# Performance work log

Measured on AMD Instinct MI355X. Metric: run time of the kernel, lower is better.

The kernel has to match this reference:

```python
import jax, jax.numpy as jnp
import numpy as np

DECAY = 0.99
BETA = 0.25
EPS_NORM = 1e-12  # matches F.normalize eps


def _l2_normalize(x):
    n = jnp.linalg.norm(x, axis=-1, keepdims=True)
    return x / jnp.maximum(n, EPS_NORM)


def setup_inputs() -> dict:
    key = jax.random.key(0)
    ks = jax.random.split(key, 8)
    B, C, H, W = 16, 256, 64, 64
    D, K = 16, 4096  # codebook_dim, n_embed
    z = jax.random.normal(ks[0], (B, C, H, W), dtype=jnp.float32)
    # 1x1 convs == per-pixel linear layers
    w_down = jax.random.normal(ks[1], (D, C), dtype=jnp.float32) / np.sqrt(C).astype(np.float32)
    b_down = jnp.zeros((D,), dtype=jnp.float32)
    w_up = jax.random.normal(ks[2], (C, D), dtype=jnp.float32) / np.sqrt(D).astype(np.float32)
    b_up = jnp.zeros((C,), dtype=jnp.float32)
    embedding = jax.random.uniform(ks[3], (K, D), minval=-1.0 / K, maxval=1.0 / K, dtype=jnp.float32)
    cluster_size = jax.random.uniform(ks[4], (K,), minval=0.5, maxval=2.0, dtype=jnp.float32)
    embed_avg = jax.random.normal(ks[5], (K, D), dtype=jnp.float32) * 0.01
    return {"z": z, "w_down": w_down, "b_down": b_down, "w_up": w_up,
            "b_up": b_up, "embedding": embedding,
            "cluster_size": cluster_size, "embed_avg": embed_avg}


def reference(z, w_down, b_down, w_up, b_up, embedding, cluster_size, embed_avg):
    B, C, H, W = z.shape
    K, D = embedding.shape

    # proj_down: 1x1 conv -> per-token linear
    z_low = jnp.einsum('bchw,dc->bdhw', z, w_down) + b_down[None, :, None, None]
    z_flat = z_low.transpose(0, 2, 3, 1).reshape(-1, D)          # [N, D]
    z_norm = _l2_normalize(z_flat)
    e_norm = _l2_normalize(embedding)                             # [K, D]

    # squared L2 distances (argmin identical to cdist argmin)
    d2 = (jnp.sum(z_norm * z_norm, -1, keepdims=True)
          - 2.0 * z_norm @ e_norm.T
          + jnp.sum(e_norm * e_norm, -1)[None, :])               # [N, K]
    indices = jnp.argmin(d2, axis=-1)                             # [N]
    z_q_flat = e_norm[indices]                                    # [N, D]

    # EMA buffer update (training path); scatter-accumulate via segment_sum
    ones = jnp.ones(indices.shape, dtype=jnp.float32)
    batch_cluster_size = jax.ops.segment_sum(ones, indices, num_segments=K)
    batch_embed_sum = jax.ops.segment_sum(z_norm, indices, num_segments=K)
    new_cluster_size = cluster_size * DECAY + (1.0 - DECAY) * batch_cluster_size
    new_embed_avg = embed_avg * DECAY + (1.0 - DECAY) * batch_embed_sum
    n = new_cluster_size.sum()
    cs = (new_cluster_size + 1e-5) / (n + K * 1e-5) * n
    new_embedding = new_embed_avg / cs[:, None]

    commitment_loss = BETA * jnp.mean((z_norm - jax.lax.stop_gradient(z_q_flat)) ** 2)

    # straight-through estimator
    z_q_low_flat = z_norm + jax.lax.stop_gradient(z_q_flat - z_norm)
    z_q_low = z_q_low_flat.reshape(B, H, W, D).transpose(0, 3, 1, 2)
    z_q = jnp.einsum('bdhw,cd->bchw', z_q_low, w_up) + b_up[None, :, None, None]

    indices_2d = indices.reshape(B, H, W)

    # metrics / entropy loss (usage == bincount(indices))
    usage_prob = batch_cluster_size / (batch_cluster_size.sum() + 1e-8)
    entropy = -jnp.sum(usage_prob * jnp.log(usage_prob + 1e-8))
    entropy_loss = jnp.log(jnp.float32(K)) - entropy

    return (z_q, commitment_loss, indices_2d, entropy_loss,
            new_embedding, new_cluster_size, new_embed_avg)
```

## Files before the change

### kernel.cpp

```cpp
#include <hip/hip_runtime.h>
#include <math.h>

#define NTOK 65536
#define CDIM 256
#define DDIM 16
#define KCOD 4096
#define HWSZ 4096

#define KSPLIT 16
#define CPS (KCOD / KSPLIT)
#define TPT 8
#define TBLK (256 * TPT)

#define WS_ENORM 0
#define WS_ENN   (WS_ENORM + KCOD*DDIM)
#define WS_ZN    (WS_ENN + KCOD)
#define WS_ZNN   (WS_ZN + NTOK*DDIM)
#define WS_BCS   (WS_ZNN + NTOK)
#define WS_BES   (WS_BCS + KCOD)
#define WS_SCAL  (WS_BES + KCOD*DDIM)
#define WS_PACK  (WS_SCAL + 8)

#define OFS_ZQ   0
#define OFS_LOSS 16777216
#define OFS_IDX  16777217
#define OFS_ENT  16842753
#define OFS_NE   16842754
#define OFS_NCS  16908290
#define OFS_NEA  16912386

__global__ __launch_bounds__(256) void knorm_kernel(const float* __restrict__ emb,
                                                    float* __restrict__ ws) {
  int k = blockIdx.x * 256 + threadIdx.x;
  const float4* src = (const float4*)emb + (size_t)k * 4;
  float4 t0 = src[0], t1 = src[1], t2 = src[2], t3 = src[3];
  float e[16] = {t0.x,t0.y,t0.z,t0.w, t1.x,t1.y,t1.z,t1.w,
                 t2.x,t2.y,t2.z,t2.w, t3.x,t3.y,t3.z,t3.w};
  float ss = 0.f;
  #pragma unroll
  for (int d = 0; d < 16; ++d) ss += e[d] * e[d];
  float dn = fmaxf(sqrtf(ss), 1e-12f);
  #pragma unroll
  for (int d = 0; d < 16; ++d) e[d] = e[d] / dn;
  float s2 = 0.f;
  #pragma unroll
  for (int d = 0; d < 16; ++d) s2 += e[d] * e[d];
  float4* dst = (float4*)(ws + WS_ENORM) + (size_t)k * 4;
  dst[0] = make_float4(e[0],e[1],e[2],e[3]);
  dst[1] = make_float4(e[4],e[5],e[6],e[7]);
  dst[2] = make_float4(e[8],e[9],e[10],e[11]);
  dst[3] = make_float4(e[12],e[13],e[14],e[15]);
  ws[WS_ENN + k] = s2;
}

__global__ __launch_bounds__(256) void kdown_kernel(const float* __restrict__ z,
                                                    const float* __restrict__ w_down,
                                                    const float* __restrict__ b_down,
                                                    float* __restrict__ ws) {
  __shared__ float wdT[CDIM * DDIM];
  const int tid = threadIdx.x;
  const int n = blockIdx.x * 256 + tid;
  const int b = n >> 12;
  const int hw = n & 4095;

  for (int i = tid; i < CDIM * DDIM; i += 256) {
    int d = i >> 8, c = i & 255;
    wdT[c * 16 + d] = w_down[i];
  }
  __syncthreads();

  const float* zp = z + (size_t)b * (CDIM * HWSZ) + hw;
  float acc[16];
  #pragma unroll
  for (int d = 0; d < 16; ++d) acc[d] = 0.f;
  #pragma unroll 16
  for (int c = 0; c < CDIM; ++c) {
    float zv = zp[(size_t)c * HWSZ];
    const float4* wr = (const float4*)(wdT + c * 16);
    float4 w0 = wr[0], w1 = wr[1], w2 = wr[2], w3 = wr[3];
    acc[0]  = fmaf(zv, w0.x, acc[0]);  acc[1]  = fmaf(zv, w0.y, acc[1]);
    acc[2]  = fmaf(zv, w0.z, acc[2]);  acc[3]  = fmaf(zv, w0.w, acc[3]);
    acc[4]  = fmaf(zv, w1.x, acc[4]);  acc[5]  = fmaf(zv, w1.y, acc[5]);
    acc[6]  = fmaf(zv, w1.z, acc[6]);  acc[7]  = fmaf(zv, w1.w, acc[7]);
    acc[8]  = fmaf(zv, w2.x, acc[8]);  acc[9]  = fmaf(zv, w2.y, acc[9]);
    acc[10] = fmaf(zv, w2.z, acc[10]); acc[11] = fmaf(zv, w2.w, acc[11]);
    acc[12] = fmaf(zv, w3.x, acc[12]); acc[13] = fmaf(zv, w3.y, acc[13]);
    acc[14] = fmaf(zv, w3.z, acc[14]); acc[15] = fmaf(zv, w3.w, acc[15]);
  }
  #pragma unroll
  for (int d = 0; d < 16; ++d) acc[d] = acc[d] + b_down[d];
  float ss = 0.f;
  #pragma unroll
  for (int d = 0; d < 16; ++d) ss += acc[d] * acc[d];
  float dn = fmaxf(sqrtf(ss), 1e-12f);
  float zn[16];
  #pragma unroll
  for (int d = 0; d < 16; ++d) zn[d] = acc[d] / dn;
  float znn = 0.f;
  {
    float sq[16];
    #pragma unroll
    for (int d = 0; d < 16; ++d) sq[d] = zn[d] * zn[d];
    #pragma unroll
    for (int d = 0; d < 16; ++d) znn += sq[d];
  }
  float4* op = (float4*)(ws + WS_ZN) + (size_t)n * 4;
  op[0] = make_float4(zn[0],zn[1],zn[2],zn[3]);
  op[1] = make_float4(zn[4],zn[5],zn[6],zn[7]);
  op[2] = make_float4(zn[8],zn[9],zn[10],zn[11]);
  op[3] = make_float4(zn[12],zn[13],zn[14],zn[15]);
  ws[WS_ZNN + n] = znn;
}

__global__ __launch_bounds__(256) void kscan_kernel(float* __restrict__ ws) {
  __shared__ float ecache[CPS * DDIM];
  __shared__ float encache[CPS];

  const int tid = threadIdx.x;
  const int kbase = blockIdx.y * CPS;

  {
    const float4* s4 = (const float4*)(ws + WS_ENORM + (size_t)kbase * 16);
    float4* d4 = (float4*)ecache;
    #pragma unroll
    for (int i = 0; i < 4; ++i) d4[tid + i * 256] = s4[tid + i * 256];
    encache[tid] = ws[WS_ENN + kbase + tid];
  }
  __syncthreads();

  float zn[TPT][16];
  float znn[TPT], best[TPT];
  int bidx[TPT];
  const int tokbase = blockIdx.x * TBLK + tid;
  {
    const float4* zp = (const float4*)(ws + WS_ZN);
    #pragma unroll
    for (int p = 0; p < TPT; ++p) {
      int tok = tokbase + p * 256;
      float4 a0 = zp[(size_t)tok * 4 + 0];
      float4 a1 = zp[(size_t)tok * 4 + 1];
      float4 a2 = zp[(size_t)tok * 4 + 2];
      float4 a3 = zp[(size_t)tok * 4 + 3];
      zn[p][0]=a0.x; zn[p][1]=a0.y; zn[p][2]=a0.z; zn[p][3]=a0.w;
      zn[p][4]=a1.x; zn[p][5]=a1.y; zn[p][6]=a1.z; zn[p][7]=a1.w;
      zn[p][8]=a2.x; zn[p][9]=a2.y; zn[p][10]=a2.z; zn[p][11]=a2.w;
      zn[p][12]=a3.x; zn[p][13]=a3.y; zn[p][14]=a3.z; zn[p][15]=a3.w;
      znn[p] = ws[WS_ZNN + tok];
      best[p] = 3.4e38f;
      bidx[p] = 0;
    }
  }

  #pragma unroll 2
  for (int j = 0; j < CPS; ++j) {
    const float4* e4 = (const float4*)(ecache + j * 16);
    float4 c0 = e4[0], c1 = e4[1], c2 = e4[2], c3 = e4[3];
    float en = encache[j];
    #pragma unroll
    for (int p = 0; p < TPT; ++p) {
      float d = 0.f;
      d = fmaf(zn[p][0],  c0.x, d); d = fmaf(zn[p][1],  c0.y, d);
      d = fmaf(zn[p][2],  c0.z, d); d = fmaf(zn[p][3],  c0.w, d);
      d = fmaf(zn[p][4],  c1.x, d); d = fmaf(zn[p][5],  c1.y, d);
      d = fmaf(zn[p][6],  c1.z, d); d = fmaf(zn[p][7],  c1.w, d);
      d = fmaf(zn[p][8],  c2.x, d); d = fmaf(zn[p][9],  c2.y, d);
      d = fmaf(zn[p][10], c2.z, d); d = fmaf(zn[p][11], c2.w, d);
      d = fmaf(zn[p][12], c3.x, d); d = fmaf(zn[p][13], c3.y, d);
      d = fmaf(zn[p][14], c3.z, d); d = fmaf(zn[p][15], c3.w, d);
      float sc = fmaf(-2.0f, d, znn[p]) + en;
      if (sc < best[p]) { best[p] = sc; bidx[p] = j; }
    }
  }

  unsigned long long* packp = (unsigned long long*)(ws + WS_PACK);
  #pragma unroll
  for (int p = 0; p < TPT; ++p) {
    int tok = tokbase + p * 256;
    unsigned u = __float_as_uint(best[p]);
    u = (u & 0x80000000u) ? ~u : (u | 0x80000000u);
    unsigned long long key =
        ((unsigned long long)u << 32) | (unsigned)(kbase + bidx[p]);
    atomicMin(packp + tok, key);
  }
}

__global__ __launch_bounds__(256) void kfinal_kernel(const float* __restrict__ w_up,
                                                     const float* __restrict__ b_up,
                                                     float* __restrict__ ws,
                                                     float* __restrict__ out) {
  __shared__ float wu[CDIM * DDIM];
  __shared__ float bu[CDIM];
  const int tid = threadIdx.x;
  {
    const float4* s4 = (const float4*)w_up;
    float4* d4 = (float4*)wu;
    #pragma unroll
    for (int i = 0; i < 4; ++i) d4[tid + i * 256] = s4[tid + i * 256];
    bu[tid] = b_up[tid];
  }
  __syncthreads();

  const int n = blockIdx.x * 256 + tid;
  const unsigned long long* packp = (const unsigned long long*)(ws + WS_PACK);
  const int bidx = (int)(unsigned)(packp[n] & 0xFFFFFFFFull);

  float zn[16];
  {
    const float4* zp = (const float4*)(ws + WS_ZN) + (size_t)n * 4;
    float4 a0 = zp[0], a1 = zp[1], a2 = zp[2], a3 = zp[3];
    zn[0]=a0.x; zn[1]=a0.y; zn[2]=a0.z; zn[3]=a0.w;
    zn[4]=a1.x; zn[5]=a1.y; zn[6]=a1.z; zn[7]=a1.w;
    zn[8]=a2.x; zn[9]=a2.y; zn[10]=a2.z; zn[11]=a2.w;
    zn[12]=a3.x; zn[13]=a3.y; zn[14]=a3.z; zn[15]=a3.w;
  }
  float zq[16];
  {
    const float4* eb = (const float4*)(ws + WS_ENORM) + (size_t)bidx * 4;
    float4 q0 = eb[0], q1 = eb[1], q2 = eb[2], q3 = eb[3];
    zq[0]=q0.x; zq[1]=q0.y; zq[2]=q0.z; zq[3]=q0.w;
    zq[4]=q1.x; zq[5]=q1.y; zq[6]=q1.z; zq[7]=q1.w;
    zq[8]=q2.x; zq[9]=q2.y; zq[10]=q2.z; zq[11]=q2.w;
    zq[12]=q3.x; zq[13]=q3.y; zq[14]=q3.z; zq[15]=q3.w;
  }

  out[OFS_IDX + n] = (float)bidx;

  float ls = 0.f;
  #pragma unroll
  for (int d = 0; d < 16; ++d) { float df = zn[d] - zq[d]; ls = fmaf(df, df, ls); }

  atomicAdd(ws + WS_BCS + bidx, 1.0f);
  #pragma unroll
  for (int d = 0; d < 16; ++d) atomicAdd(ws + WS_BES + (size_t)bidx * 16 + d, zn[d]);

  #pragma unroll
  for (int off = 32; off > 0; off >>= 1) ls += __shfl_down(ls, off, 64);
  if ((tid & 63) == 0) atomicAdd(ws + WS_SCAL + 0, ls);

  float ql[16];
  #pragma unroll
  for (int d = 0; d < 16; ++d) ql[d] = zn[d] + (zq[d] - zn[d]);

  const int b = n >> 12, hw = n & 4095;
  float* op = out + OFS_ZQ + (size_t)b * (CDIM * HWSZ) + hw;
  #pragma unroll 4
  for (int c = 0; c < CDIM; ++c) {
    const float4* wr = (const float4*)(wu + c * 16);
    float4 w0 = wr[0], w1 = wr[1], w2 = wr[2], w3 = wr[3];
    float a = 0.f;
    a = fmaf(ql[0],  w0.x, a); a = fmaf(ql[1],  w0.y, a);
    a = fmaf(ql[2],  w0.z, a); a = fmaf(ql[3],  w0.w, a);
    a = fmaf(ql[4],  w1.x, a); a = fmaf(ql[5],  w1.y, a);
    a = fmaf(ql[6],  w1.z, a); a = fmaf(ql[7],  w1.w, a);
    a = fmaf(ql[8],  w2.x, a); a = fmaf(ql[9],  w2.y, a);
    a = fmaf(ql[10], w2.z, a); a = fmaf(ql[11], w2.w, a);
    a = fmaf(ql[12], w3.x, a); a = fmaf(ql[13], w3.y, a);
    a = fmaf(ql[14], w3.z, a); a = fmaf(ql[15], w3.w, a);
    a = a + bu[c];
    op[(size_t)c * HWSZ] = a;
  }
}

__global__ __launch_bounds__(256) void kema_kernel(const float* __restrict__ cluster_size,
                                                   const float* __restrict__ embed_avg,
                                                   float* __restrict__ ws,
                                                   float* __restrict__ out) {
  const float DEC = 0.99f;
  const float OMD = (float)(1.0 - 0.99);
  const int k = blockIdx.x * 256 + threadIdx.x;
  float bcsv = ws[WS_BCS + k];
  float ncs = cluster_size[k] * DEC + OMD * bcsv;
  out[OFS_NCS + k] = ncs;
  #pragma unroll
  for (int d = 0; d < 16; ++d) {
    float nea = embed_avg[(size_t)k * 16 + d] * DEC + OMD * ws[WS_BES + (size_t)k * 16 + d];
    out[OFS_NEA + (size_t)k * 16 + d] = nea;
  }
  float p = bcsv / 65536.0f;
  float et = -p * logf(p + 1e-8f);

  __shared__ float r1[4], r2[4];
  float v1 = ncs, v2 = et;
  #pragma unroll
  for (int off = 32; off > 0; off >>= 1) {
    v1 += __shfl_down(v1, off, 64);
    v2 += __shfl_down(v2, off, 64);
  }
  int lane = threadIdx.x & 63, w = threadIdx.x >> 6;
  if (lane == 0) { r1[w] = v1; r2[w] = v2; }
  __syncthreads();
  if (threadIdx.x == 0) {
    atomicAdd(ws + WS_SCAL + 1, (r1[0] + r1[1]) + (r1[2] + r1[3]));
    atomicAdd(ws + WS_SCAL + 2, (r2[0] + r2[1]) + (r2[2] + r2[3]));
  }
}

__global__ __launch_bounds__(64) void kscal_kernel(const float* __restrict__ ws,
                                                   float* __restrict__ out) {
  if (threadIdx.x == 0) {
    out[OFS_LOSS] = 0.25f * (ws[WS_SCAL + 0] / 1048576.0f);
    out[OFS_ENT]  = (float)8.317766166719343 - ws[WS_SCAL + 2];
  }
}

__global__ __launch_bounds__(256) void kemb_kernel(const float* __restrict__ ws,
                                                   float* __restrict__ out) {
  const float KEPS = (float)(4096.0 * 1e-5);
  const int k = blockIdx.x * 256 + threadIdx.x;
  float n = ws[WS_SCAL + 1];
  float ncs = out[OFS_NCS + k];
  float cs = (ncs + 1e-5f) / (n + KEPS) * n;
  #pragma unroll
  for (int d = 0; d < 16; ++d)
    out[OFS_NE + (size_t)k * 16 + d] = out[OFS_NEA + (size_t)k * 16 + d] / cs;
}

extern "C" void kernel_launch(void* const* d_in, const int* in_sizes, int n_in,
                              void* d_out, int out_size, void* d_ws, size_t ws_size,
                              hipStream_t stream) {
  const float* z        = (const float*)d_in[0];
  const float* w_down   = (const float*)d_in[1];
  const float* b_down   = (const float*)d_in[2];
  const float* w_up     = (const float*)d_in[3];
  const float* b_up     = (const float*)d_in[4];
  const float* emb      = (const float*)d_in[5];
  const float* csz      = (const float*)d_in[6];
  const float* eavg     = (const float*)d_in[7];
  float* out = (float*)d_out;
  float* ws  = (float*)d_ws;

  hipMemsetAsync(ws + WS_BCS, 0, (size_t)(KCOD + KCOD*DDIM + 8) * sizeof(float), stream);
  hipMemsetAsync(ws + WS_PACK, 0xFF, (size_t)NTOK * 8, stream);

  knorm_kernel<<<KCOD / 256, 256, 0, stream>>>(emb, ws);
  kdown_kernel<<<NTOK / 256, 256, 0, stream>>>(z, w_down, b_down, ws);
  kscan_kernel<<<dim3(NTOK / TBLK, KSPLIT), 256, 0, stream>>>(ws);
  kfinal_kernel<<<NTOK / 256, 256, 0, stream>>>(w_up, b_up, ws, out);
  kema_kernel<<<KCOD / 256, 256, 0, stream>>>(csz, eavg, ws, out);
  kscal_kernel<<<1, 64, 0, stream>>>(ws, out);
  kemb_kernel<<<KCOD / 256, 256, 0, stream>>>(ws, out);
}
```

Before: 247.9 us.

## Restructure VQ kernels: drop shared staging, fold -2 and norm into scan, merge scalar kernel

The w_down transpose moves into the codebook-normalize kernel and is stored in workspace, so the down-projection reads it from global/cached memory and no longer stages it through LDS with a barrier. The w_up LDS staging in the final kernel is likewise removed. The scan kernel drops the per-token norm term, which is constant across codes and does not change the argmin, and pre-scales z by -2 so the distance becomes a single FMA chain seeded with the code norm. Tokens per thread drop from 8 to 4 with a launch_bounds occupancy hint, and the tiny scalar kernel is merged into the embedding kernel to save a launch. The main risk is that lower register reuse per thread in the scan, or uncoalesced broadcast global reads in place of LDS, could cost more than they save.

After: 271.6 us. +9.5%, slower.

```diff
diff --git a/kernel.cpp b/kernel.cpp
--- a/kernel.cpp
+++ b/kernel.cpp
@@ -9,14 +9,14 @@
 
 #define KSPLIT 16
 #define CPS (KCOD / KSPLIT)
-#define TPT 8
+#define TPT 4
 #define TBLK (256 * TPT)
 
 #define WS_ENORM 0
 #define WS_ENN   (WS_ENORM + KCOD*DDIM)
-#define WS_ZN    (WS_ENN + KCOD)
-#define WS_ZNN   (WS_ZN + NTOK*DDIM)
-#define WS_BCS   (WS_ZNN + NTOK)
+#define WS_WDT   (WS_ENN + KCOD)
+#define WS_ZN    (WS_WDT + CDIM*DDIM)
+#define WS_BCS   (WS_ZN + NTOK*DDIM)
 #define WS_BES   (WS_BCS + KCOD)
 #define WS_SCAL  (WS_BES + KCOD*DDIM)
 #define WS_PACK  (WS_SCAL + 8)
@@ -30,6 +30,7 @@
 #define OFS_NEA  16912386
 
 __global__ __launch_bounds__(256) void knorm_kernel(const float* __restrict__ emb,
+                                                    const float* __restrict__ w_down,
                                                     float* __restrict__ ws) {
   int k = blockIdx.x * 256 + threadIdx.x;
   const float4* src = (const float4*)emb + (size_t)k * 4;
@@ -51,32 +52,26 @@
   dst[2] = make_float4(e[8],e[9],e[10],e[11]);
   dst[3] = make_float4(e[12],e[13],e[14],e[15]);
   ws[WS_ENN + k] = s2;
+  ws[WS_WDT + k] = w_down[(k & 15) * 256 + (k >> 4)];
 }
 
 __global__ __launch_bounds__(256) void kdown_kernel(const float* __restrict__ z,
-                                                    const float* __restrict__ w_down,
+                                                    const float* __restrict__ wdt,
                                                     const float* __restrict__ b_down,
-                                                    float* __restrict__ ws) {
-  __shared__ float wdT[CDIM * DDIM];
+                                                    float* __restrict__ znp) {
   const int tid = threadIdx.x;
   const int n = blockIdx.x * 256 + tid;
   const int b = n >> 12;
   const int hw = n & 4095;
 
-  for (int i = tid; i < CDIM * DDIM; i += 256) {
-    int d = i >> 8, c = i & 255;
-    wdT[c * 16 + d] = w_down[i];
-  }
-  __syncthreads();
-
   const float* zp = z + (size_t)b * (CDIM * HWSZ) + hw;
   float acc[16];
   #pragma unroll
   for (int d = 0; d < 16; ++d) acc[d] = 0.f;
-  #pragma unroll 16
+  #pragma unroll 8
   for (int c = 0; c < CDIM; ++c) {
     float zv = zp[(size_t)c * HWSZ];
-    const float4* wr = (const float4*)(wdT + c * 16);
+    const float4* wr = (const float4*)(wdt + c * 16);
     float4 w0 = wr[0], w1 = wr[1], w2 = wr[2], w3 = wr[3];
     acc[0]  = fmaf(zv, w0.x, acc[0]);  acc[1]  = fmaf(zv, w0.y, acc[1]);
     acc[2]  = fmaf(zv, w0.z, acc[2]);  acc[3]  = fmaf(zv, w0.w, acc[3]);
@@ -96,23 +91,18 @@
   float zn[16];
   #pragma unroll
   for (int d = 0; d < 16; ++d) zn[d] = acc[d] / dn;
-  float znn = 0.f;
-  {
-    float sq[16];
-    #pragma unroll
-    for (int d = 0; d < 16; ++d) sq[d] = zn[d] * zn[d];
-    #pragma unroll
-    for (int d = 0; d < 16; ++d) znn += sq[d];
-  }
-  float4* op = (float4*)(ws + WS_ZN) + (size_t)n * 4;
+
+  float4* op = (float4*)znp + (size_t)n * 4;
   op[0] = make_float4(zn[0],zn[1],zn[2],zn[3]);
   op[1] = make_float4(zn[4],zn[5],zn[6],zn[7]);
   op[2] = make_float4(zn[8],zn[9],zn[10],zn[11]);
   op[3] = make_float4(zn[12],zn[13],zn[14],zn[15]);
-  ws[WS_ZNN + n] = znn;
-}
-
-__global__ __launch_bounds__(256) void kscan_kernel(float* __restrict__ ws) {
+}
+
+__global__ __launch_bounds__(256, 4) void kscan_kernel(const float* __restrict__ enorm,
+                                                       const float* __restrict__ ennp,
+                                                       const float* __restrict__ znp,
+                                                       unsigned long long* __restrict__ packp) {
   __shared__ float ecache[CPS * DDIM];
   __shared__ float encache[CPS];
 
@@ -120,20 +110,20 @@
   const int kbase = blockIdx.y * CPS;
 
   {
-    const float4* s4 = (const float4*)(ws + WS_ENORM + (size_t)kbase * 16);
+    const float4* s4 = (const float4*)(enorm + (size_t)kbase * 16);
     float4* d4 = (float4*)ecache;
     #pragma unroll
     for (int i = 0; i < 4; ++i) d4[tid + i * 256] = s4[tid + i * 256];
-    encache[tid] = ws[WS_ENN + kbase + tid];
+    encache[tid] = ennp[kbase + tid];
   }
   __syncthreads();
 
-  float zn[TPT][16];
-  float znn[TPT], best[TPT];
+  float nz[TPT][16];
+  float best[TPT];
   int bidx[TPT];
   const int tokbase = blockIdx.x * TBLK + tid;
   {
-    const float4* zp = (const float4*)(ws + WS_ZN);
+    const float4* zp = (const float4*)znp;
     #pragma unroll
     for (int p = 0; p < TPT; ++p) {
       int tok = tokbase + p * 256;
@@ -141,11 +131,10 @@
       float4 a1 = zp[(size_t)tok * 4 + 1];
       float4 a2 = zp[(size_t)tok * 4 + 2];
       float4 a3 = zp[(size_t)tok * 4 + 3];
-      zn[p][0]=a0.x; zn[p][1]=a0.y; zn[p][2]=a0.z; zn[p][3]=a0.w;
-      zn[p][4]=a1.x; zn[p][5]=a1.y; zn[p][6]=a1.z; zn[p][7]=a1.w;
-      zn[p][8]=a2.x; zn[p][9]=a2.y; zn[p][10]=a2.z; zn[p][11]=a2.w;
-      zn[p][12]=a3.x; zn[p][13]=a3.y; zn[p][14]=a3.z; zn[p][15]=a3.w;
-      znn[p] = ws[WS_ZNN + tok];
+      nz[p][0]=-2.f*a0.x; nz[p][1]=-2.f*a0.y; nz[p][2]=-2.f*a0.z; nz[p][3]=-2.f*a0.w;
+      nz[p][4]=-2.f*a1.x; nz[p][5]=-2.f*a1.y; nz[p][6]=-2.f*a1.z; nz[p][7]=-2.f*a1.w;
+      nz[p][8]=-2.f*a2.x; nz[p][9]=-2.f*a2.y; nz[p][10]=-2.f*a2.z; nz[p][11]=-2.f*a2.w;
+      nz[p][12]=-2.f*a3.x; nz[p][13]=-2.f*a3.y; nz[p][14]=-2.f*a3.z; nz[p][15]=-2.f*a3.w;
       best[p] = 3.4e38f;
       bidx[p] = 0;
     }
@@ -158,21 +147,19 @@
     float en = encache[j];
     #pragma unroll
     for (int p = 0; p < TPT; ++p) {
-      float d = 0.f;
-      d = fmaf(zn[p][0],  c0.x, d); d = fmaf(zn[p][1],  c0.y, d);
-      d = fmaf(zn[p][2],  c0.z, d); d = fmaf(zn[p][3],  c0.w, d);
-      d = fmaf(zn[p][4],  c1.x, d); d = fmaf(zn[p][5],  c1.y, d);
-      d = fmaf(zn[p][6],  c1.z, d); d = fmaf(zn[p][7],  c1.w, d);
-      d = fmaf(zn[p][8],  c2.x, d); d = fmaf(zn[p][9],  c2.y, d);
-      d = fmaf(zn[p][10], c2.z, d); d = fmaf(zn[p][11], c2.w, d);
-      d = fmaf(zn[p][12], c3.x, d); d = fmaf(zn[p][13], c3.y, d);
-      d = fmaf(zn[p][14], c3.z, d); d = fmaf(zn[p][15], c3.w, d);
-      float sc = fmaf(-2.0f, d, znn[p]) + en;
-      if (sc < best[p]) { best[p] = sc; bidx[p] = j; }
+      float d = en;
+      d = fmaf(nz[p][0],  c0.x, d); d = fmaf(nz[p][1],  c0.y, d);
+      d = fmaf(nz[p][2],  c0.z, d); d = fmaf(nz[p][3],  c0.w, d);
+      d = fmaf(nz[p][4],  c1.x, d); d = fmaf(nz[p][5],  c1.y, d);
+      d = fmaf(nz[p][6],  c1.z, d); d = fmaf(nz[p][7],  c1.w, d);
+      d = fmaf(nz[p][8],  c2.x, d); d = fmaf(nz[p][9],  c2.y, d);
+      d = fmaf(nz[p][10], c2.z, d); d = fmaf(nz[p][11], c2.w, d);
+      d = fmaf(nz[p][12], c3.x, d); d = fmaf(nz[p][13], c3.y, d);
+      d = fmaf(nz[p][14], c3.z, d); d = fmaf(nz[p][15], c3.w, d);
+      if (d < best[p]) { best[p] = d; bidx[p] = j; }
     }
   }
 
-  unsigned long long* packp = (unsigned long long*)(ws + WS_PACK);
   #pragma unroll
   for (int p = 0; p < TPT; ++p) {
     int tok = tokbase + p * 256;
@@ -186,27 +173,18 @@
 
 __global__ __launch_bounds__(256) void kfinal_kernel(const float* __restrict__ w_up,
                                                      const float* __restrict__ b_up,
-                                                     float* __restrict__ ws,
+                                                     const float* __restrict__ enorm,
+                                                     const float* __restrict__ znp,
+                                                     const unsigned long long* __restrict__ packp,
+                                                     float* __restrict__ wsacc,
                                                      float* __restrict__ out) {
-  __shared__ float wu[CDIM * DDIM];
-  __shared__ float bu[CDIM];
   const int tid = threadIdx.x;
-  {
-    const float4* s4 = (const float4*)w_up;
-    float4* d4 = (float4*)wu;
-    #pragma unroll
-    for (int i = 0; i < 4; ++i) d4[tid + i * 256] = s4[tid + i * 256];
-    bu[tid] = b_up[tid];
-  }
-  __syncthreads();
-
   const int n = blockIdx.x * 256 + tid;
-  const unsigned long long* packp = (const unsigned long long*)(ws + WS_PACK);
   const int bidx = (int)(unsigned)(packp[n] & 0xFFFFFFFFull);
 
   float zn[16];
   {
-    const float4* zp = (const float4*)(ws + WS_ZN) + (size_t)n * 4;
+    const float4* zp = (const float4*)znp + (size_t)n * 4;
     float4 a0 = zp[0], a1 = zp[1], a2 = zp[2], a3 = zp[3];
     zn[0]=a0.x; zn[1]=a0.y; zn[2]=a0.z; zn[3]=a0.w;
     zn[4]=a1.x; zn[5]=a1.y; zn[6]=a1.z; zn[7]=a1.w;
@@ -215,7 +193,7 @@
   }
   float zq[16];
   {
-    const float4* eb = (const float4*)(ws + WS_ENORM) + (size_t)bidx * 4;
+    const float4* eb = (const float4*)enorm + (size_t)bidx * 4;
     float4 q0 = eb[0], q1 = eb[1], q2 = eb[2], q3 = eb[3];
     zq[0]=q0.x; zq[1]=q0.y; zq[2]=q0.z; zq[3]=q0.w;
     zq[4]=q1.x; zq[5]=q1.y; zq[6]=q1.z; zq[7]=q1.w;
@@ -229,13 +207,14 @@
   #pragma unroll
   for (int d = 0; d < 16; ++d) { float df = zn[d] - zq[d]; ls = fmaf(df, df, ls); }
 
-  atomicAdd(ws + WS_BCS + bidx, 1.0f);
-  #pragma unroll
-  for (int d = 0; d < 16; ++d) atomicAdd(ws + WS_BES + (size_t)bidx * 16 + d, zn[d]);
+  atomicAdd(wsacc + WS_BCS - WS_BCS + bidx, 1.0f);
+  #pragma unroll
+  for (int d = 0; d < 16; ++d)
+    atomicAdd(wsacc + KCOD + (size_t)bidx * 16 + d, zn[d]);
 
   #pragma unroll
   for (int off = 32; off > 0; off >>= 1) ls += __shfl_down(ls, off, 64);
-  if ((tid & 63) == 0) atomicAdd(ws + WS_SCAL + 0, ls);
+  if ((tid & 63) == 0) atomicAdd(wsacc + KCOD + KCOD * DDIM + 0, ls);
 
   float ql[16];
   #pragma unroll
@@ -243,9 +222,9 @@
 
   const int b = n >> 12, hw = n & 4095;
   float* op = out + OFS_ZQ + (size_t)b * (CDIM * HWSZ) + hw;
-  #pragma unroll 4
+  #pragma unroll 8
   for (int c = 0; c < CDIM; ++c) {
-    const float4* wr = (const float4*)(wu + c * 16);
+    const float4* wr = (const float4*)(w_up + c * 16);
     float4 w0 = wr[0], w1 = wr[1], w2 = wr[2], w3 = wr[3];
     float a = 0.f;
     a = fmaf(ql[0],  w0.x, a); a = fmaf(ql[1],  w0.y, a);
@@ -256,7 +235,7 @@
     a = fmaf(ql[10], w2.z, a); a = fmaf(ql[11], w2.w, a);
     a = fmaf(ql[12], w3.x, a); a = fmaf(ql[13], w3.y, a);
     a = fmaf(ql[14], w3.z, a); a = fmaf(ql[15], w3.w, a);
-    a = a + bu[c];
+    a = a + b_up[c];
     op[(size_t)c * HWSZ] = a;
   }
 }
@@ -295,14 +274,6 @@
   }
 }
 
-__global__ __launch_bounds__(64) void kscal_kernel(const float* __restrict__ ws,
-                                                   float* __restrict__ out) {
-  if (threadIdx.x == 0) {
-    out[OFS_LOSS] = 0.25f * (ws[WS_SCAL + 0] / 1048576.0f);
-    out[OFS_ENT]  = (float)8.317766166719343 - ws[WS_SCAL + 2];
-  }
-}
-
 __global__ __launch_bounds__(256) void kemb_kernel(const float* __restrict__ ws,
                                                    float* __restrict__ out) {
   const float KEPS = (float)(4096.0 * 1e-5);
@@ -313,6 +284,10 @@
   #pragma unroll
   for (int d = 0; d < 16; ++d)
     out[OFS_NE + (size_t)k * 16 + d] = out[OFS_NEA + (size_t)k * 16 + d] / cs;
+  if (k == 0) {
+    out[OFS_LOSS] = 0.25f * (ws[WS_SCAL + 0] / 1048576.0f);
+    out[OFS_ENT]  = (float)8.317766166719343 - ws[WS_SCAL + 2];
+  }
 }
 
 extern "C" void kernel_launch(void* const* d_in, const int* in_sizes, int n_in,
@@ -332,11 +307,14 @@
   hipMemsetAsync(ws + WS_BCS, 0, (size_t)(KCOD + KCOD*DDIM + 8) * sizeof(float), stream);
   hipMemsetAsync(ws + WS_PACK, 0xFF, (size_t)NTOK * 8, stream);
 
-  knorm_kernel<<<KCOD / 256, 256, 0, stream>>>(emb, ws);
-  kdown_kernel<<<NTOK / 256, 256, 0, stream>>>(z, w_down, b_down, ws);
-  kscan_kernel<<<dim3(NTOK / TBLK, KSPLIT), 256, 0, stream>>>(ws);
-  kfinal_kernel<<<NTOK / 256, 256, 0, stream>>>(w_up, b_up, ws, out);
+  knorm_kernel<<<KCOD / 256, 256, 0, stream>>>(emb, w_down, ws);
+  kdown_kernel<<<NTOK / 256, 256, 0, stream>>>(z, ws + WS_WDT, b_down, ws + WS_ZN);
+  kscan_kernel<<<dim3(NTOK / TBLK, KSPLIT), 256, 0, stream>>>(
+      ws + WS_ENORM, ws + WS_ENN, ws + WS_ZN,
+      (unsigned long long*)(ws + WS_PACK));
+  kfinal_kernel<<<NTOK / 256, 256, 0, stream>>>(
+      w_up, b_up, ws + WS_ENORM, ws + WS_ZN,
+      (const unsigned long long*)(ws + WS_PACK), ws + WS_BCS, out);
   kema_kernel<<<KCOD / 256, 256, 0, stream>>>(csz, eavg, ws, out);
-  kscal_kernel<<<1, 64, 0, stream>>>(ws, out);
   kemb_kernel<<<KCOD / 256, 256, 0, stream>>>(ws, out);
 }
```
